# Performance work log

Hardware: AMD Instinct MI355X
Metric: run time of the kernel (lower is better)

## Reference

```python
import jax, jax.numpy as jnp
import numpy as np

NEG_SLOPE = 0.2


def _gat_layer(x, src, dst, W, att_src, att_dst, bias, concat):
    # x: [N, Fin], W: [Fin, H*C], att_*: [H, C], bias: [H*C] or [C]
    N = x.shape[0]
    H, C = att_src.shape
    h = (x @ W).reshape(N, H, C)                      # node features per head
    a_src = jnp.sum(h * att_src, axis=-1)             # [N, H]
    a_dst = jnp.sum(h * att_dst, axis=-1)             # [N, H]
    e = jax.nn.leaky_relu(a_src[src] + a_dst[dst], NEG_SLOPE)  # [E, H]
    # segment softmax over destination nodes
    m = jax.ops.segment_max(e, dst, num_segments=N)   # [N, H]
    m = jnp.where(jnp.isfinite(m), m, 0.0)
    ex = jnp.exp(e - m[dst])
    s = jax.ops.segment_sum(ex, dst, num_segments=N)  # [N, H]
    alpha = ex / (s[dst] + 1e-16)                     # [E, H]
    msg = h[src] * alpha[:, :, None]                  # [E, H, C]
    out = jax.ops.segment_sum(msg, dst, num_segments=N)  # [N, H, C]
    out = out.reshape(N, H * C) if concat else out.mean(axis=1)
    return out + bias


def setup_inputs() -> dict:
    key = jax.random.key(0)
    ks = jax.random.split(key, 20)
    N, E, Fin, Cg, H = 50000, 800000, 128, 64, 4
    HC = H * Cg
    s = 0.1
    x = jax.random.normal(ks[0], (N, Fin), jnp.float32)
    edge_index = jax.random.randint(ks[1], (2, E), 0, N, dtype=jnp.int32)
    inp = {
        'x': x,
        'edge_index': edge_index,
        'W0': jax.random.normal(ks[2], (Fin, HC), jnp.float32) * s,
        'as0': jax.random.normal(ks[3], (H, Cg), jnp.float32) * s,
        'ad0': jax.random.normal(ks[4], (H, Cg), jnp.float32) * s,
        'b0': jnp.zeros((HC,), jnp.float32),
        'W1': jax.random.normal(ks[5], (HC, HC), jnp.float32) * s,
        'as1': jax.random.normal(ks[6], (H, Cg), jnp.float32) * s,
        'ad1': jax.random.normal(ks[7], (H, Cg), jnp.float32) * s,
        'b1': jnp.zeros((HC,), jnp.float32),
        'W2': jax.random.normal(ks[8], (HC, HC), jnp.float32) * s,
        'as2': jax.random.normal(ks[9], (H, Cg), jnp.float32) * s,
        'ad2': jax.random.normal(ks[10], (H, Cg), jnp.float32) * s,
        'b2': jnp.zeros((Cg,), jnp.float32),
        # linear head: 64 -> 128 -> 10
        'lw0': jax.random.normal(ks[11], (Cg, 128), jnp.float32) * s,
        'lb0': jnp.zeros((128,), jnp.float32),
        'lw1': jax.random.normal(ks[12], (128, 10), jnp.float32) * s,
        'lb1': jnp.zeros((10,), jnp.float32),
    }
    return inp


def reference(x, edge_index, W0, as0, ad0, b0, W1, as1, ad1, b1,
              W2, as2, ad2, b2, lw0, lb0, lw1, lb1):
    N = x.shape[0]
    # PyG GATConv add_self_loops=True: append self-loop edges
    loop = jnp.arange(N, dtype=edge_index.dtype)
    src = jnp.concatenate([edge_index[0], loop])
    dst = jnp.concatenate([edge_index[1], loop])
    h = _gat_layer(x, src, dst, W0, as0, ad0, b0, True)
    h = _gat_layer(h, src, dst, W1, as1, ad1, b1, True)
    h = _gat_layer(h, src, dst, W2, as2, ad2, b2, False)
    h = jax.nn.relu(h @ lw0 + lb0)
    return h @ lw1 + lb1
```

## Files before the change

### kernel.cpp

```cpp
#include <hip/hip_runtime.h>
#include <hip/hip_bf16.h>

#define HEADS 4
#define CH 64
#define HC 256

typedef __attribute__((ext_vector_type(8))) short short8;
typedef __attribute__((ext_vector_type(4))) float f32x4;
typedef __attribute__((ext_vector_type(8))) _Float16 half8;

__device__ inline unsigned short f2bf(float f){
  unsigned u = __float_as_uint(f);
  return (unsigned short)((u + 0x7FFF + ((u >> 16) & 1)) >> 16);
}


__global__ void hist_kernel(const int* __restrict__ dst, int E, int ET, int* __restrict__ cnt){
  int e = blockIdx.x * blockDim.x + threadIdx.x;
  if (e >= ET) return;
  int d = (e < E) ? dst[e] : (e - E);
  atomicAdd(&cnt[d], 1);
}

__global__ void blocksum_kernel(const int* __restrict__ cnt, int N, int* __restrict__ bsum){
  int tid = threadIdx.x;
  int i = blockIdx.x * 256 + tid;
  int v = (i < N) ? cnt[i] : 0;
  #pragma unroll
  for (int off = 32; off >= 1; off >>= 1) v += __shfl_xor(v, off);
  __shared__ int ws[4];
  if ((tid & 63) == 0) ws[tid >> 6] = v;
  __syncthreads();
  if (tid == 0) bsum[blockIdx.x] = ws[0] + ws[1] + ws[2] + ws[3];
}

__global__ void scanb_kernel(int* __restrict__ bsum, int nb){
  __shared__ int buf[256];
  int tid = threadIdx.x;
  int v = (tid < nb) ? bsum[tid] : 0;
  buf[tid] = v;
  __syncthreads();
  #pragma unroll
  for (int off = 1; off < 256; off <<= 1){
    int t = (tid >= off) ? buf[tid - off] : 0;
    __syncthreads();
    buf[tid] += t;
    __syncthreads();
  }
  if (tid < nb) bsum[tid] = buf[tid] - v;
}

__global__ void scanfinal_kernel(const int* __restrict__ cnt, const int* __restrict__ bsum,
                                 int* __restrict__ ptr, int* __restrict__ cur, int N){
  __shared__ int buf[256];
  int tid = threadIdx.x;
  int i = blockIdx.x * 256 + tid;
  int v = (i < N) ? cnt[i] : 0;
  buf[tid] = v;
  __syncthreads();
  #pragma unroll
  for (int off = 1; off < 256; off <<= 1){
    int t = (tid >= off) ? buf[tid - off] : 0;
    __syncthreads();
    buf[tid] += t;
    __syncthreads();
  }
  int exc = buf[tid] - v + bsum[blockIdx.x];
  if (i < N){
    ptr[i] = exc; cur[i] = exc;
    if (i == N - 1) ptr[N] = exc + v;
  }
}

__global__ void scatter_kernel(const int* __restrict__ src, const int* __restrict__ dst,
                               int E, int ET, int* __restrict__ cur, int* __restrict__ csr_src){
  int e = blockIdx.x * blockDim.x + threadIdx.x;
  if (e >= ET) return;
  int s, d;
  if (e < E){ s = src[e]; d = dst[e]; } else { s = e - E; d = e - E; }
  int pos = atomicAdd(&cur[d], 1);
  csr_src[pos] = s;
}


__global__ void wsplit_kernel(const float* __restrict__ W0, unsigned short* __restrict__ h0,
                              unsigned short* __restrict__ l0,
                              const float* __restrict__ W1, unsigned short* __restrict__ h1,
                              unsigned short* __restrict__ l1,
                              const float* __restrict__ W2, unsigned short* __restrict__ h2,
                              unsigned short* __restrict__ l2){
  int idx = blockIdx.x * 256 + threadIdx.x;
  const float* W; unsigned short *hi, *lo; int K;
  if (idx < 128 * HC){ W = W0; hi = h0; lo = l0; K = 128; }
  else if (idx < (128 + 256) * HC){ idx -= 128 * HC; W = W1; hi = h1; lo = l1; K = 256; }
  else { idx -= (128 + 256) * HC; W = W2; hi = h2; lo = l2; K = 256; }
  int k = idx >> 8, n = idx & 255;
  float w = W[idx];
  unsigned short hb = f2bf(w);
  float hf = __uint_as_float((unsigned)hb << 16);
  unsigned short lb = f2bf(w - hf);
  hi[(size_t)n * K + k] = hb;
  lo[(size_t)n * K + k] = lb;
}


__global__ void xsplit_kernel(const float* __restrict__ x, int total4,
                              unsigned short* __restrict__ xhi, unsigned short* __restrict__ xlo){
  int i4 = blockIdx.x * 256 + threadIdx.x;
  if (i4 >= total4) return;
  float4 v = *(const float4*)&x[(size_t)i4 * 4];
  float va[4] = {v.x, v.y, v.z, v.w};
  unsigned short h4[4], l4[4];
  #pragma unroll
  for (int j = 0; j < 4; j++){
    unsigned short hb = f2bf(va[j]);
    float hf = __uint_as_float((unsigned)hb << 16);
    h4[j] = hb;
    l4[j] = f2bf(va[j] - hf);
  }
  *(ushort4*)&xhi[(size_t)i4 * 4] = make_ushort4(h4[0], h4[1], h4[2], h4[3]);
  *(ushort4*)&xlo[(size_t)i4 * 4] = make_ushort4(l4[0], l4[1], l4[2], l4[3]);
}


__global__ void lwsplit_kernel(const float* __restrict__ lw0,
                               unsigned short* __restrict__ l0hi, unsigned short* __restrict__ l0lo,
                               const float* __restrict__ lw1, _Float16* __restrict__ l1T){
  int idx = blockIdx.x * 256 + threadIdx.x;
  if (idx < 8192){
    int n = idx & 127, k = idx >> 7;
    float w = lw0[k * 128 + n];
    unsigned short hb = f2bf(w);
    float hf = __uint_as_float((unsigned)hb << 16);
    unsigned short lb = f2bf(w - hf);
    l0hi[n * 64 + k] = hb;
    l0lo[n * 64 + k] = lb;
  } else if (idx < 8192 + 2048){
    int id = idx - 8192;
    int n = id & 15, k = id >> 4;
    float w = (n < 10) ? lw1[k * 10 + n] : 0.f;
    l1T[n * 128 + k] = (_Float16)w;
  }
}


__launch_bounds__(256, 2)
__global__ void gemm_mfma_kernel(const unsigned short* __restrict__ Ahi,
                                 const unsigned short* __restrict__ Alo,
                                 const unsigned short* __restrict__ BhiT,
                                 const unsigned short* __restrict__ BloT,
                                 _Float16* __restrict__ Cm,
                                 const float* __restrict__ att_s, const float* __restrict__ att_d,
                                 float* __restrict__ a_src, float* __restrict__ a_dst,
                                 int M, int K){
  __shared__ unsigned short As_hi[128][40];
  __shared__ unsigned short As_lo[128][40];
  __shared__ unsigned short Bs_hi[128][40];
  __shared__ unsigned short Bs_lo[128][40];

  int tid = threadIdx.x;
  int m0 = blockIdx.x * 128, n0 = blockIdx.y * 128;
  int wave = tid >> 6, lane = tid & 63;
  int wm = (wave >> 1) * 64, wn = (wave & 1) * 64;
  int col = lane & 15, quad = lane >> 4;

  f32x4 acc[4][4];
  #pragma unroll
  for (int a = 0; a < 4; a++)
    #pragma unroll
    for (int b = 0; b < 4; b++)
      acc[a][b] = (f32x4){0.f, 0.f, 0.f, 0.f};

  const short8 zero8 = (short8){0,0,0,0,0,0,0,0};

  for (int k0 = 0; k0 < K; k0 += 32){
    #pragma unroll
    for (int r = 0; r < 2; r++){
      int id = r * 256 + tid;
      int m = id >> 2, q = id & 3;
      int gm = m0 + m;
      size_t g = (size_t)gm * K + k0 + q * 8;
      short8 vh = zero8, vl = zero8;
      if (gm < M){
        vh = *(const short8*)&Ahi[g];
        vl = *(const short8*)&Alo[g];
      }
      *(short8*)&As_hi[m][q * 8] = vh;
      *(short8*)&As_lo[m][q * 8] = vl;
    }
    #pragma unroll
    for (int r = 0; r < 2; r++){
      int id = r * 256 + tid;
      int n = id >> 2, q = id & 3;
      size_t g = (size_t)(n0 + n) * K + k0 + q * 8;
      *(short8*)&Bs_hi[n][q * 8] = *(const short8*)&BhiT[g];
      *(short8*)&Bs_lo[n][q * 8] = *(const short8*)&BloT[g];
    }
    __syncthreads();

    short8 af[4][2], bf[4][2];
    #pragma unroll
    for (int t = 0; t < 4; t++){
      af[t][0] = *(const short8*)&As_hi[wm + t * 16 + col][quad * 8];
      af[t][1] = *(const short8*)&As_lo[wm + t * 16 + col][quad * 8];
      bf[t][0] = *(const short8*)&Bs_hi[wn + t * 16 + col][quad * 8];
      bf[t][1] = *(const short8*)&Bs_lo[wn + t * 16 + col][quad * 8];
    }
    #pragma unroll
    for (int mt = 0; mt < 4; mt++)
      #pragma unroll
      for (int nt = 0; nt < 4; nt++){
        acc[mt][nt] = __builtin_amdgcn_mfma_f32_16x16x32_bf16(af[mt][0], bf[nt][0], acc[mt][nt], 0, 0, 0);
        acc[mt][nt] = __builtin_amdgcn_mfma_f32_16x16x32_bf16(af[mt][1], bf[nt][0], acc[mt][nt], 0, 0, 0);
        acc[mt][nt] = __builtin_amdgcn_mfma_f32_16x16x32_bf16(af[mt][0], bf[nt][1], acc[mt][nt], 0, 0, 0);
      }
    __syncthreads();
  }

  #pragma unroll
  for (int mt = 0; mt < 4; mt++)
    #pragma unroll
    for (int nt = 0; nt < 4; nt++){
      int colg = n0 + wn + nt * 16 + col;
      #pragma unroll
      for (int r = 0; r < 4; r++){
        int row = m0 + wm + mt * 16 + quad * 4 + r;
        if (row < M) Cm[(size_t)row * HC + colg] = (_Float16)acc[mt][nt][r];
      }
    }

  int head = (n0 + wn) >> 6;
  float asv[4], adv[4];
  #pragma unroll
  for (int nt = 0; nt < 4; nt++){
    asv[nt] = att_s[head * CH + nt * 16 + col];
    adv[nt] = att_d[head * CH + nt * 16 + col];
  }
  #pragma unroll
  for (int mt = 0; mt < 4; mt++){
    float sp[4] = {0.f,0.f,0.f,0.f}, dp[4] = {0.f,0.f,0.f,0.f};
    #pragma unroll
    for (int nt = 0; nt < 4; nt++)
      #pragma unroll
      for (int r = 0; r < 4; r++){
        sp[r] += acc[mt][nt][r] * asv[nt];
        dp[r] += acc[mt][nt][r] * adv[nt];
      }
    #pragma unroll
    for (int off = 1; off <= 8; off <<= 1)
      #pragma unroll
      for (int r = 0; r < 4; r++){
        sp[r] += __shfl_xor(sp[r], off);
        dp[r] += __shfl_xor(dp[r], off);
      }
    if (col == 0){
      #pragma unroll
      for (int r = 0; r < 4; r++){
        int row = m0 + wm + mt * 16 + quad * 4 + r;
        if (row < M){
          a_src[row * HEADS + head] = sp[r];
          a_dst[row * HEADS + head] = dp[r];
        }
      }
    }
  }
}


__global__ void agg_kernel(const _Float16* __restrict__ h, const float* __restrict__ a_src,
                           const float* __restrict__ a_dst, const int* __restrict__ ptr,
                           const int* __restrict__ csr_src, const float* __restrict__ bias,
                           unsigned short* __restrict__ out_hi, unsigned short* __restrict__ out_lo,
                           int N, int mean_mode, const float* __restrict__ b2,
                           float* __restrict__ f2){
  __shared__ float sm[HEADS][CH];
  int n = blockIdx.x;
  int head = threadIdx.x >> 6;
  int lane = threadIdx.x & 63;
  int eg = lane >> 3, c8 = lane & 7;
  int beg = ptr[n], end = ptr[n + 1];
  float adst = a_dst[n * HEADS + head];

  float acc0[8] = {0.f,0.f,0.f,0.f,0.f,0.f,0.f,0.f};
  float acc1[8] = {0.f,0.f,0.f,0.f,0.f,0.f,0.f,0.f};
  float ss0 = 0.f, ss1 = 0.f;
  int i = beg + eg;
  for (; i + 8 < end; i += 16){
    int s0 = csr_src[i], s1 = csr_src[i + 8];
    float e0 = a_src[s0 * HEADS + head] + adst;
    float e1 = a_src[s1 * HEADS + head] + adst;
    e0 = e0 > 0.f ? e0 : 0.2f * e0;
    e1 = e1 > 0.f ? e1 : 0.2f * e1;
    float w0 = __expf(e0), w1 = __expf(e1);
    half8 h0 = *(const half8*)&h[(size_t)s0 * HC + head * CH + c8 * 8];
    half8 h1 = *(const half8*)&h[(size_t)s1 * HC + head * CH + c8 * 8];
    #pragma unroll
    for (int j = 0; j < 8; j++){
      acc0[j] += w0 * (float)h0[j];
      acc1[j] += w1 * (float)h1[j];
    }
    ss0 += w0; ss1 += w1;
  }
  if (i < end){
    int s0 = csr_src[i];
    float e0 = a_src[s0 * HEADS + head] + adst;
    e0 = e0 > 0.f ? e0 : 0.2f * e0;
    float w0 = __expf(e0);
    half8 h0 = *(const half8*)&h[(size_t)s0 * HC + head * CH + c8 * 8];
    #pragma unroll
    for (int j = 0; j < 8; j++) acc0[j] += w0 * (float)h0[j];
    ss0 += w0;
  }
  float ss = ss0 + ss1;
  float acc[8];
  #pragma unroll
  for (int j = 0; j < 8; j++) acc[j] = acc0[j] + acc1[j];
  #pragma unroll
  for (int off = 8; off <= 32; off <<= 1){
    #pragma unroll
    for (int j = 0; j < 8; j++) acc[j] += __shfl_xor(acc[j], off);
    ss += __shfl_xor(ss, off);
  }
  float inv = 1.f / (ss + 1e-16f);
  #pragma unroll
  for (int j = 0; j < 8; j++) acc[j] *= inv;

  if (!mean_mode){
    if (eg == 0){
      const float* bp = &bias[head * CH + c8 * 8];
      short8 hi8, lo8;
      #pragma unroll
      for (int j = 0; j < 8; j++){
        float v = acc[j] + bp[j];
        unsigned short hb = f2bf(v);
        float hf = __uint_as_float((unsigned)hb << 16);
        hi8[j] = (short)hb;
        lo8[j] = (short)f2bf(v - hf);
      }
      size_t o = (size_t)n * HC + head * CH + c8 * 8;
      *(short8*)&out_hi[o] = hi8;
      *(short8*)&out_lo[o] = lo8;
    }
  } else {
    if (eg == 0){
      #pragma unroll
      for (int j = 0; j < 8; j++) sm[head][c8 * 8 + j] = acc[j];
    }
    __syncthreads();
    int t = threadIdx.x;
    if (t < CH)
      f2[(size_t)n * CH + t] =
        0.25f * (sm[0][t] + sm[1][t] + sm[2][t] + sm[3][t]) + b2[t];
  }
}


__launch_bounds__(256, 2)
__global__ void head_mfma_kernel(const float* __restrict__ f2,
                                 const unsigned short* __restrict__ lw0hiT,
                                 const unsigned short* __restrict__ lw0loT,
                                 const _Float16* __restrict__ lw1T,
                                 const float* __restrict__ lb0,
                                 const float* __restrict__ lb1,
                                 float* __restrict__ outp, int N){
  __shared__ __align__(16) unsigned short L[27648];
  __shared__ __align__(16) _Float16 Ls[16][136];
  const int tid = threadIdx.x;
  const int wave = tid >> 6, lane = tid & 63;
  const int col = lane & 15, quad = lane >> 4;
  const int m0 = blockIdx.x * 64;

  { int n = tid >> 4, k = (tid & 15) * 8;
    *(half8*)&Ls[n][k] = *(const half8*)&lw1T[n * 128 + k]; }

  #pragma unroll
  for (int r = 0; r < 2; r++){
    int id = r * 256 + tid;
    int m = id >> 3, q = id & 7;
    int gm = m0 + m;
    float va[8];
    if (gm < N){
      float4 v0 = *(const float4*)&f2[(size_t)gm * CH + q * 8];
      float4 v1 = *(const float4*)&f2[(size_t)gm * CH + q * 8 + 4];
      va[0]=v0.x; va[1]=v0.y; va[2]=v0.z; va[3]=v0.w;
      va[4]=v1.x; va[5]=v1.y; va[6]=v1.z; va[7]=v1.w;
    } else {
      #pragma unroll
      for (int j = 0; j < 8; j++) va[j] = 0.f;
    }
    short8 hi8, lo8;
    #pragma unroll
    for (int j = 0; j < 8; j++){
      unsigned short hb = f2bf(va[j]);
      float hf = __uint_as_float((unsigned)hb << 16);
      hi8[j] = (short)hb;
      lo8[j] = (short)f2bf(va[j] - hf);
    }
    *(short8*)&L[m * 72 + q * 8] = hi8;
    *(short8*)&L[4608 + m * 72 + q * 8] = lo8;
  }
  #pragma unroll
  for (int r = 0; r < 4; r++){
    int id = r * 256 + tid;
    int n = id >> 3, q = id & 7;
    *(short8*)&L[9216 + n * 72 + q * 8]  = *(const short8*)&lw0hiT[n * 64 + q * 8];
    *(short8*)&L[18432 + n * 72 + q * 8] = *(const short8*)&lw0loT[n * 64 + q * 8];
  }
  __syncthreads();

  const int wn = wave * 32;
  f32x4 acc[4][2];
  #pragma unroll
  for (int a = 0; a < 4; a++)
    #pragma unroll
    for (int b = 0; b < 2; b++) acc[a][b] = (f32x4){0.f,0.f,0.f,0.f};

  #pragma unroll
  for (int ks = 0; ks < 2; ks++){
    int k = ks * 32 + quad * 8;
    short8 ah[4], al[4], bh[2], bl[2];
    #pragma unroll
    for (int mt = 0; mt < 4; mt++){
      ah[mt] = *(short8*)&L[(mt * 16 + col) * 72 + k];
      al[mt] = *(short8*)&L[4608 + (mt * 16 + col) * 72 + k];
    }
    #pragma unroll
    for (int nt = 0; nt < 2; nt++){
      bh[nt] = *(short8*)&L[9216 + (wn + nt * 16 + col) * 72 + k];
      bl[nt] = *(short8*)&L[18432 + (wn + nt * 16 + col) * 72 + k];
    }
    #pragma unroll
    for (int mt = 0; mt < 4; mt++)
      #pragma unroll
      for (int nt = 0; nt < 2; nt++){
        acc[mt][nt] = __builtin_amdgcn_mfma_f32_16x16x32_bf16(ah[mt], bh[nt], acc[mt][nt], 0, 0, 0);
        acc[mt][nt] = __builtin_amdgcn_mfma_f32_16x16x32_bf16(al[mt], bh[nt], acc[mt][nt], 0, 0, 0);
        acc[mt][nt] = __builtin_amdgcn_mfma_f32_16x16x32_bf16(ah[mt], bl[nt], acc[mt][nt], 0, 0, 0);
      }
  }
  __syncthreads();

  _Float16* Zp = (_Float16*)L;
  #pragma unroll
  for (int nt = 0; nt < 2; nt++){
    int n = wn + nt * 16 + col;
    float b = lb0[n];
    #pragma unroll
    for (int mt = 0; mt < 4; mt++)
      #pragma unroll
      for (int r2 = 0; r2 < 4; r2++){
        int m = mt * 16 + quad * 4 + r2;
        float z = acc[mt][nt][r2] + b;
        Zp[m * 136 + n] = (_Float16)fmaxf(z, 0.f);
      }
  }
  __syncthreads();

  f32x4 acc2 = (f32x4){0.f,0.f,0.f,0.f};
  #pragma unroll
  for (int ks = 0; ks < 4; ks++){
    int k = ks * 32 + quad * 8;
    half8 a2 = *(half8*)&Zp[(wave * 16 + col) * 136 + k];
    half8 b2v = *(half8*)&Ls[col][k];
    acc2 = __builtin_amdgcn_mfma_f32_16x16x32_f16(a2, b2v, acc2, 0, 0, 0);
  }
  if (col < 10){
    float bb = lb1[col];
    #pragma unroll
    for (int r2 = 0; r2 < 4; r2++){
      int row = m0 + wave * 16 + quad * 4 + r2;
      if (row < N) outp[(size_t)row * 10 + col] = acc2[r2] + bb;
    }
  }
}


extern "C" void kernel_launch(void* const* d_in, const int* in_sizes, int n_in,
                              void* d_out, int out_size, void* d_ws, size_t ws_size,
                              hipStream_t stream) {
  const float* x   = (const float*)d_in[0];
  const int*   ei  = (const int*)d_in[1];
  const float* W0  = (const float*)d_in[2];
  const float* as0 = (const float*)d_in[3];
  const float* ad0 = (const float*)d_in[4];
  const float* b0  = (const float*)d_in[5];
  const float* W1  = (const float*)d_in[6];
  const float* as1 = (const float*)d_in[7];
  const float* ad1 = (const float*)d_in[8];
  const float* b1  = (const float*)d_in[9];
  const float* W2  = (const float*)d_in[10];
  const float* as2 = (const float*)d_in[11];
  const float* ad2 = (const float*)d_in[12];
  const float* b2  = (const float*)d_in[13];
  const float* lw0 = (const float*)d_in[14];
  const float* lb0 = (const float*)d_in[15];
  const float* lw1 = (const float*)d_in[16];
  const float* lb1 = (const float*)d_in[17];
  float* outp = (float*)d_out;

  int N  = in_sizes[0] / 128;
  int E  = in_sizes[1] / 2;
  int ET = E + N;
  int nb = (N + 255) / 256;

  char* ws = (char*)d_ws;
  _Float16* Hb = (_Float16*)ws;       ws += (size_t)N * HC * sizeof(_Float16);
  unsigned short* Fhi = (unsigned short*)ws; ws += (size_t)N * HC * 2;
  unsigned short* Flo = (unsigned short*)ws; ws += (size_t)N * HC * 2;
  float* f2  = (float*)ws; ws += (size_t)N * CH * sizeof(float);
  float* a_s = (float*)ws; ws += (size_t)N * HEADS * sizeof(float);
  float* a_d = (float*)ws; ws += (size_t)N * HEADS * sizeof(float);
  int* cnt   = (int*)ws;   ws += (size_t)N * sizeof(int);
  int* cur   = (int*)ws;   ws += (size_t)N * sizeof(int);
  int* ptrA  = (int*)ws;   ws += (size_t)(N + 1) * sizeof(int);
  int* bsum  = (int*)ws;   ws += (size_t)nb * sizeof(int);
  int* csr   = (int*)ws;   ws += (size_t)ET * sizeof(int);
  unsigned short* w0hi = (unsigned short*)ws; ws += (size_t)128 * HC * 2;
  unsigned short* w0lo = (unsigned short*)ws; ws += (size_t)128 * HC * 2;
  unsigned short* w1hi = (unsigned short*)ws; ws += (size_t)HC * HC * 2;
  unsigned short* w1lo = (unsigned short*)ws; ws += (size_t)HC * HC * 2;
  unsigned short* w2hi = (unsigned short*)ws; ws += (size_t)HC * HC * 2;
  unsigned short* w2lo = (unsigned short*)ws; ws += (size_t)HC * HC * 2;
  unsigned short* l0hi = (unsigned short*)ws; ws += (size_t)8192 * 2;
  unsigned short* l0lo = (unsigned short*)ws; ws += (size_t)8192 * 2;
  _Float16* l1T        = (_Float16*)ws;       ws += (size_t)2048 * 2;

  const int* srcArr = ei;
  const int* dstArr = ei + E;

  hipMemsetAsync(cnt, 0, (size_t)N * sizeof(int), stream);
  hist_kernel<<<(ET + 255) / 256, 256, 0, stream>>>(dstArr, E, ET, cnt);
  blocksum_kernel<<<nb, 256, 0, stream>>>(cnt, N, bsum);
  scanb_kernel<<<1, 256, 0, stream>>>(bsum, nb);
  scanfinal_kernel<<<nb, 256, 0, stream>>>(cnt, bsum, ptrA, cur, N);
  scatter_kernel<<<(ET + 255) / 256, 256, 0, stream>>>(srcArr, dstArr, E, ET, cur, csr);

  wsplit_kernel<<<((128 + 256 + 256) * HC) / 256, 256, 0, stream>>>(
      W0, w0hi, w0lo, W1, w1hi, w1lo, W2, w2hi, w2lo);
  lwsplit_kernel<<<(8192 + 2048 + 255) / 256, 256, 0, stream>>>(lw0, l0hi, l0lo, lw1, l1T);
  xsplit_kernel<<<(N * 128 / 4 + 255) / 256, 256, 0, stream>>>(x, N * 128 / 4, Fhi, Flo);

  dim3 ggrid((N + 127) / 128, 2);

  gemm_mfma_kernel<<<ggrid, 256, 0, stream>>>(Fhi, Flo, w0hi, w0lo, Hb, as0, ad0, a_s, a_d, N, 128);
  agg_kernel<<<N, 256, 0, stream>>>(Hb, a_s, a_d, ptrA, csr, b0, Fhi, Flo, N, 0, nullptr, nullptr);

  gemm_mfma_kernel<<<ggrid, 256, 0, stream>>>(Fhi, Flo, w1hi, w1lo, Hb, as1, ad1, a_s, a_d, N, HC);
  agg_kernel<<<N, 256, 0, stream>>>(Hb, a_s, a_d, ptrA, csr, b1, Fhi, Flo, N, 0, nullptr, nullptr);

  gemm_mfma_kernel<<<ggrid, 256, 0, stream>>>(Fhi, Flo, w2hi, w2lo, Hb, as2, ad2, a_s, a_d, N, HC);
  agg_kernel<<<N, 256, 0, stream>>>(Hb, a_s, a_d, ptrA, csr, nullptr, nullptr, nullptr, N, 1, b2, f2);

  head_mfma_kernel<<<(N + 63) / 64, 256, 0, stream>>>(f2, l0hi, l0lo, l1T, lb0, lb1, outp, N);
}
```

Measured before the change: 593.8 us.

## Precompute per-edge attention weights in separate kernel; pad GEMM rows to remove bounds checks

```diff
diff --git a/kernel.cpp b/kernel.cpp
--- a/kernel.cpp
+++ b/kernel.cpp
@@ -73,13 +73,33 @@
 }
 
 __global__ void scatter_kernel(const int* __restrict__ src, const int* __restrict__ dst,
-                               int E, int ET, int* __restrict__ cur, int* __restrict__ csr_src){
+                               int E, int ET, int* __restrict__ cur,
+                               int* __restrict__ csr_src, int* __restrict__ csr_dst){
   int e = blockIdx.x * blockDim.x + threadIdx.x;
   if (e >= ET) return;
   int s, d;
   if (e < E){ s = src[e]; d = dst[e]; } else { s = e - E; d = e - E; }
   int pos = atomicAdd(&cur[d], 1);
   csr_src[pos] = s;
+  csr_dst[pos] = d;
+}
+
+
+__global__ void ew_kernel(const int* __restrict__ csr_src, const int* __restrict__ csr_dst,
+                          const float* __restrict__ a_src, const float* __restrict__ a_dst,
+                          float* __restrict__ w, int ET){
+  int i = blockIdx.x * 256 + threadIdx.x;
+  if (i >= ET) return;
+  int s = csr_src[i], d = csr_dst[i];
+  float4 as = *(const float4*)&a_src[(size_t)s * 4];
+  float4 ad = *(const float4*)&a_dst[(size_t)d * 4];
+  float4 r;
+  float e;
+  e = as.x + ad.x; e = e > 0.f ? e : 0.2f * e; r.x = __expf(e);
+  e = as.y + ad.y; e = e > 0.f ? e : 0.2f * e; r.y = __expf(e);
+  e = as.z + ad.z; e = e > 0.f ? e : 0.2f * e; r.z = __expf(e);
+  e = as.w + ad.w; e = e > 0.f ? e : 0.2f * e; r.w = __expf(e);
+  *(float4*)&w[(size_t)i * 4] = r;
 }
 
 
@@ -152,7 +172,7 @@
                                  _Float16* __restrict__ Cm,
                                  const float* __restrict__ att_s, const float* __restrict__ att_d,
                                  float* __restrict__ a_src, float* __restrict__ a_dst,
-                                 int M, int K){
+                                 int K){
   __shared__ unsigned short As_hi[128][40];
   __shared__ unsigned short As_lo[128][40];
   __shared__ unsigned short Bs_hi[128][40];
@@ -171,22 +191,14 @@
     for (int b = 0; b < 4; b++)
       acc[a][b] = (f32x4){0.f, 0.f, 0.f, 0.f};
 
-  const short8 zero8 = (short8){0,0,0,0,0,0,0,0};
-
   for (int k0 = 0; k0 < K; k0 += 32){
     #pragma unroll
     for (int r = 0; r < 2; r++){
       int id = r * 256 + tid;
       int m = id >> 2, q = id & 3;
-      int gm = m0 + m;
-      size_t g = (size_t)gm * K + k0 + q * 8;
-      short8 vh = zero8, vl = zero8;
-      if (gm < M){
-        vh = *(const short8*)&Ahi[g];
-        vl = *(const short8*)&Alo[g];
-      }
-      *(short8*)&As_hi[m][q * 8] = vh;
-      *(short8*)&As_lo[m][q * 8] = vl;
+      size_t g = (size_t)(m0 + m) * K + k0 + q * 8;
+      *(short8*)&As_hi[m][q * 8] = *(const short8*)&Ahi[g];
+      *(short8*)&As_lo[m][q * 8] = *(const short8*)&Alo[g];
     }
     #pragma unroll
     for (int r = 0; r < 2; r++){
@@ -225,7 +237,7 @@
       #pragma unroll
       for (int r = 0; r < 4; r++){
         int row = m0 + wm + mt * 16 + quad * 4 + r;
-        if (row < M) Cm[(size_t)row * HC + colg] = (_Float16)acc[mt][nt][r];
+        Cm[(size_t)row * HC + colg] = (_Float16)acc[mt][nt][r];
       }
     }
 
@@ -257,19 +269,17 @@
       #pragma unroll
       for (int r = 0; r < 4; r++){
         int row = m0 + wm + mt * 16 + quad * 4 + r;
-        if (row < M){
-          a_src[row * HEADS + head] = sp[r];
-          a_dst[row * HEADS + head] = dp[r];
-        }
-      }
-    }
-  }
-}
-
-
-__global__ void agg_kernel(const _Float16* __restrict__ h, const float* __restrict__ a_src,
-                           const float* __restrict__ a_dst, const int* __restrict__ ptr,
-                           const int* __restrict__ csr_src, const float* __restrict__ bias,
+        a_src[row * HEADS + head] = sp[r];
+        a_dst[row * HEADS + head] = dp[r];
+      }
+    }
+  }
+}
+
+
+__global__ void agg_kernel(const _Float16* __restrict__ h, const float* __restrict__ w,
+                           const int* __restrict__ ptr, const int* __restrict__ csr_src,
+                           const float* __restrict__ bias,
                            unsigned short* __restrict__ out_hi, unsigned short* __restrict__ out_lo,
                            int N, int mean_mode, const float* __restrict__ b2,
                            float* __restrict__ f2){
@@ -279,7 +289,6 @@
   int lane = threadIdx.x & 63;
   int eg = lane >> 3, c8 = lane & 7;
   int beg = ptr[n], end = ptr[n + 1];
-  float adst = a_dst[n * HEADS + head];
 
   float acc0[8] = {0.f,0.f,0.f,0.f,0.f,0.f,0.f,0.f};
   float acc1[8] = {0.f,0.f,0.f,0.f,0.f,0.f,0.f,0.f};
@@ -287,11 +296,8 @@
   int i = beg + eg;
   for (; i + 8 < end; i += 16){
     int s0 = csr_src[i], s1 = csr_src[i + 8];
-    float e0 = a_src[s0 * HEADS + head] + adst;
-    float e1 = a_src[s1 * HEADS + head] + adst;
-    e0 = e0 > 0.f ? e0 : 0.2f * e0;
-    e1 = e1 > 0.f ? e1 : 0.2f * e1;
-    float w0 = __expf(e0), w1 = __expf(e1);
+    float w0 = w[(size_t)i * 4 + head];
+    float w1 = w[(size_t)(i + 8) * 4 + head];
     half8 h0 = *(const half8*)&h[(size_t)s0 * HC + head * CH + c8 * 8];
     half8 h1 = *(const half8*)&h[(size_t)s1 * HC + head * CH + c8 * 8];
     #pragma unroll
@@ -303,9 +309,7 @@
   }
   if (i < end){
     int s0 = csr_src[i];
-    float e0 = a_src[s0 * HEADS + head] + adst;
-    e0 = e0 > 0.f ? e0 : 0.2f * e0;
-    float w0 = __expf(e0);
+    float w0 = w[(size_t)i * 4 + head];
     half8 h0 = *(const half8*)&h[(size_t)s0 * HC + head * CH + c8 * 8];
     #pragma unroll
     for (int j = 0; j < 8; j++) acc0[j] += w0 * (float)h0[j];
@@ -502,19 +506,22 @@
   int E  = in_sizes[1] / 2;
   int ET = E + N;
   int nb = (N + 255) / 256;
+  int Mp = ((N + 127) / 128) * 128;
 
   char* ws = (char*)d_ws;
-  _Float16* Hb = (_Float16*)ws;       ws += (size_t)N * HC * sizeof(_Float16);
-  unsigned short* Fhi = (unsigned short*)ws; ws += (size_t)N * HC * 2;
-  unsigned short* Flo = (unsigned short*)ws; ws += (size_t)N * HC * 2;
+  _Float16* Hb = (_Float16*)ws;       ws += (size_t)Mp * HC * sizeof(_Float16);
+  unsigned short* Fhi = (unsigned short*)ws; ws += (size_t)Mp * HC * 2;
+  unsigned short* Flo = (unsigned short*)ws; ws += (size_t)Mp * HC * 2;
   float* f2  = (float*)ws; ws += (size_t)N * CH * sizeof(float);
-  float* a_s = (float*)ws; ws += (size_t)N * HEADS * sizeof(float);
-  float* a_d = (float*)ws; ws += (size_t)N * HEADS * sizeof(float);
+  float* a_s = (float*)ws; ws += (size_t)Mp * HEADS * sizeof(float);
+  float* a_d = (float*)ws; ws += (size_t)Mp * HEADS * sizeof(float);
+  float* ewt = (float*)ws; ws += (size_t)ET * HEADS * sizeof(float);
   int* cnt   = (int*)ws;   ws += (size_t)N * sizeof(int);
   int* cur   = (int*)ws;   ws += (size_t)N * sizeof(int);
   int* ptrA  = (int*)ws;   ws += (size_t)(N + 1) * sizeof(int);
   int* bsum  = (int*)ws;   ws += (size_t)nb * sizeof(int);
   int* csr   = (int*)ws;   ws += (size_t)ET * sizeof(int);
+  int* csrd  = (int*)ws;   ws += (size_t)ET * sizeof(int);
   unsigned short* w0hi = (unsigned short*)ws; ws += (size_t)128 * HC * 2;
   unsigned short* w0lo = (unsigned short*)ws; ws += (size_t)128 * HC * 2;
   unsigned short* w1hi = (unsigned short*)ws; ws += (size_t)HC * HC * 2;
@@ -533,23 +540,27 @@
   blocksum_kernel<<<nb, 256, 0, stream>>>(cnt, N, bsum);
   scanb_kernel<<<1, 256, 0, stream>>>(bsum, nb);
   scanfinal_kernel<<<nb, 256, 0, stream>>>(cnt, bsum, ptrA, cur, N);
-  scatter_kernel<<<(ET + 255) / 256, 256, 0, stream>>>(srcArr, dstArr, E, ET, cur, csr);
+  scatter_kernel<<<(ET + 255) / 256, 256, 0, stream>>>(srcArr, dstArr, E, ET, cur, csr, csrd);
 
   wsplit_kernel<<<((128 + 256 + 256) * HC) / 256, 256, 0, stream>>>(
       W0, w0hi, w0lo, W1, w1hi, w1lo, W2, w2hi, w2lo);
   lwsplit_kernel<<<(8192 + 2048 + 255) / 256, 256, 0, stream>>>(lw0, l0hi, l0lo, lw1, l1T);
   xsplit_kernel<<<(N * 128 / 4 + 255) / 256, 256, 0, stream>>>(x, N * 128 / 4, Fhi, Flo);
 
-  dim3 ggrid((N + 127) / 128, 2);
-
-  gemm_mfma_kernel<<<ggrid, 256, 0, stream>>>(Fhi, Flo, w0hi, w0lo, Hb, as0, ad0, a_s, a_d, N, 128);
-  agg_kernel<<<N, 256, 0, stream>>>(Hb, a_s, a_d, ptrA, csr, b0, Fhi, Flo, N, 0, nullptr, nullptr);
-
-  gemm_mfma_kernel<<<ggrid, 256, 0, stream>>>(Fhi, Flo, w1hi, w1lo, Hb, as1, ad1, a_s, a_d, N, HC);
-  agg_kernel<<<N, 256, 0, stream>>>(Hb, a_s, a_d, ptrA, csr, b1, Fhi, Flo, N, 0, nullptr, nullptr);
-
-  gemm_mfma_kernel<<<ggrid, 256, 0, stream>>>(Fhi, Flo, w2hi, w2lo, Hb, as2, ad2, a_s, a_d, N, HC);
-  agg_kernel<<<N, 256, 0, stream>>>(Hb, a_s, a_d, ptrA, csr, nullptr, nullptr, nullptr, N, 1, b2, f2);
+  dim3 ggrid(Mp / 128, 2);
+  int eb = (ET + 255) / 256;
+
+  gemm_mfma_kernel<<<ggrid, 256, 0, stream>>>(Fhi, Flo, w0hi, w0lo, Hb, as0, ad0, a_s, a_d, 128);
+  ew_kernel<<<eb, 256, 0, stream>>>(csr, csrd, a_s, a_d, ewt, ET);
+  agg_kernel<<<N, 256, 0, stream>>>(Hb, ewt, ptrA, csr, b0, Fhi, Flo, N, 0, nullptr, nullptr);
+
+  gemm_mfma_kernel<<<ggrid, 256, 0, stream>>>(Fhi, Flo, w1hi, w1lo, Hb, as1, ad1, a_s, a_d, HC);
+  ew_kernel<<<eb, 256, 0, stream>>>(csr, csrd, a_s, a_d, ewt, ET);
+  agg_kernel<<<N, 256, 0, stream>>>(Hb, ewt, ptrA, csr, b1, Fhi, Flo, N, 0, nullptr, nullptr);
+
+  gemm_mfma_kernel<<<ggrid, 256, 0, stream>>>(Fhi, Flo, w2hi, w2lo, Hb, as2, ad2, a_s, a_d, HC);
+  ew_kernel<<<eb, 256, 0, stream>>>(csr, csrd, a_s, a_d, ewt, ET);
+  agg_kernel<<<N, 256, 0, stream>>>(Hb, ewt, ptrA, csr, nullptr, nullptr, nullptr, N, 1, b2, f2);
 
   head_mfma_kernel<<<(N + 63) / 64, 256, 0, stream>>>(f2, l0hi, l0lo, l1T, lb0, lb1, outp, N);
 }
```

New measurement: 587.9 us. Within noise of the previous version (-1.0%).
